# Kernel tuning notes

Hardware: AMD Instinct MI355X
Metric: run time of the kernel (lower is better)

Reference implementation:

```python
import jax, jax.numpy as jnp
import numpy as np
from jax import lax

B, T, V, E, H, K = 64, 512, 30000, 256, 256, 9


def setup_inputs() -> dict:
    key = jax.random.key(0)
    ks = jax.random.split(key, 15)
    s = 0.08
    return {
        "word_inputs": jax.random.randint(ks[0], (B, T), 0, V),
        "word_seq_lengths": jax.random.randint(ks[1], (B,), 1, T + 1),
        "seq_token_label": jax.random.randint(ks[2], (B, T), 0, K),
        "word_vec": jax.random.normal(ks[3], (V, E), jnp.float32) * s,
        "W_ih_f": jax.random.normal(ks[4], (4 * H, E), jnp.float32) * s,
        "W_hh_f": jax.random.normal(ks[5], (4 * H, H), jnp.float32) * s,
        "b_f": jax.random.normal(ks[6], (4 * H,), jnp.float32) * s,
        "W_ih_b": jax.random.normal(ks[7], (4 * H, E), jnp.float32) * s,
        "W_hh_b": jax.random.normal(ks[8], (4 * H, H), jnp.float32) * s,
        "b_b": jax.random.normal(ks[9], (4 * H,), jnp.float32) * s,
        "W_out": jax.random.normal(ks[10], (K, 2 * H), jnp.float32) * s,
        "b_out": jax.random.normal(ks[11], (K,), jnp.float32) * s,
        "start_trans": jax.random.normal(ks[12], (K,), jnp.float32) * s,
        "end_trans": jax.random.normal(ks[13], (K,), jnp.float32) * s,
        "trans": jax.random.normal(ks[14], (K, K), jnp.float32) * s,
    }


def _lstm_dir(x, W_ih, W_hh, b):
    # x: [B,T,E] -> h: [B,T,H]; torch gate order (i, f, g, o)
    gx = jnp.einsum('bte,ge->btg', x, W_ih) + b  # input projection hoisted out of scan
    h0 = jnp.zeros((x.shape[0], W_hh.shape[1]), x.dtype)

    def step(carry, g_t):
        h, c = carry
        g = g_t + h @ W_hh.T
        i, f, gg, o = jnp.split(g, 4, axis=-1)
        c = jax.nn.sigmoid(f) * c + jax.nn.sigmoid(i) * jnp.tanh(gg)
        h = jax.nn.sigmoid(o) * jnp.tanh(c)
        return (h, c), h

    _, hs = lax.scan(step, (h0, h0), jnp.swapaxes(gx, 0, 1))
    return jnp.swapaxes(hs, 0, 1)


def reference(word_inputs, word_seq_lengths, seq_token_label, word_vec,
              W_ih_f, W_hh_f, b_f, W_ih_b, W_hh_b, b_b,
              W_out, b_out, start_trans, end_trans, trans):
    t_idx = jnp.arange(T)
    mask = t_idx[None, :] < word_seq_lengths[:, None]  # [B,T] bool (pack_padded semantics)
    # index map that reverses the valid prefix of each sequence (involution)
    rev_idx = jnp.where(mask, word_seq_lengths[:, None] - 1 - t_idx[None, :], t_idx[None, :])

    emb = word_vec[word_inputs]  # [B,T,E]
    h_fwd = _lstm_dir(emb, W_ih_f, W_hh_f, b_f)
    emb_rev = jnp.take_along_axis(emb, rev_idx[:, :, None], axis=1)
    h_bwd = jnp.take_along_axis(_lstm_dir(emb_rev, W_ih_b, W_hh_b, b_b), rev_idx[:, :, None], axis=1)
    feats = jnp.concatenate([h_fwd, h_bwd], axis=-1) * mask[:, :, None]  # [B,T,2H]
    emissions = feats @ W_out.T + b_out  # [B,T,K]

    mf = mask.astype(emissions.dtype)
    # ---- CRF numerator (score of gold path) ----
    emit_sc = jnp.take_along_axis(emissions, seq_token_label[:, :, None], 2)[:, :, 0]  # [B,T]
    num = start_trans[seq_token_label[:, 0]] + emit_sc[:, 0]
    trans_sc = trans[seq_token_label[:, :-1], seq_token_label[:, 1:]]  # [B,T-1]
    num = num + jnp.sum((trans_sc + emit_sc[:, 1:]) * mf[:, 1:], axis=1)
    last_tags = jnp.take_along_axis(seq_token_label, (word_seq_lengths - 1)[:, None], 1)[:, 0]
    num = num + end_trans[last_tags]

    # ---- CRF log-partition (alpha recursion) ----
    em_t = jnp.swapaxes(emissions[:, 1:], 0, 1)  # [T-1,B,K]
    mk_t = jnp.swapaxes(mask[:, 1:], 0, 1)       # [T-1,B]
    score0 = start_trans[None, :] + emissions[:, 0]  # [B,K]

    def alpha_step(score, inp):
        e_t, m_t = inp
        nxt = jax.nn.logsumexp(score[:, :, None] + trans[None], axis=1) + e_t
        return jnp.where(m_t[:, None], nxt, score), None

    scoreZ, _ = lax.scan(alpha_step, score0, (em_t, mk_t))
    denom = jax.nn.logsumexp(scoreZ + end_trans[None, :], axis=1)
    ner_loss = -jnp.mean(num - denom)  # reduction='mean' over batch, negated

    # ---- Viterbi decode ----
    def vit_step(score, inp):
        e_t, m_t = inp
        tot = score[:, :, None] + trans[None]  # [B,K,K]
        best_prev = jnp.argmax(tot, axis=1)    # [B,K]
        nxt = jnp.max(tot, axis=1) + e_t
        return jnp.where(m_t[:, None], nxt, score), best_prev

    scoreV, hist = lax.scan(vit_step, score0, (em_t, mk_t))  # hist [T-1,B,K]
    best_last = jnp.argmax(scoreV + end_trans[None, :], axis=1)  # [B]

    def back_step(cur, inp):
        h_t, m_t = inp
        new = jnp.take_along_axis(h_t, cur[:, None], 1)[:, 0]
        cur = jnp.where(m_t, new, cur)
        return cur, cur

    _, preds_rev = lax.scan(back_step, best_last, (hist[::-1], mk_t[::-1]))  # [T-1,B]
    preds = jnp.concatenate([jnp.swapaxes(preds_rev[::-1], 0, 1), best_last[:, None]], axis=1)  # [B,T]
    preds = jnp.where(mask, preds, 0)

    return ner_loss, preds, feats
```

## Files before the change

kernel.cpp:

```cpp
#include <hip/hip_runtime.h>
#include <hip/hip_bf16.h>
#include <math.h>

#ifndef __has_builtin
#define __has_builtin(x) 0
#endif

typedef unsigned int uint;
typedef unsigned short ushort;
typedef _Float16 half2_t __attribute__((ext_vector_type(2)));

#define PREG 90
#define WREG_UINTS (PREG * 2 * 512)
#define WLDS_UINTS (19 * 512 * 4)

__device__ __forceinline__ float sigm(float x) {
    return __fdividef(1.0f, 1.0f + __expf(-x));
}
__device__ __forceinline__ float tanh_fast(float x) {
    float sg = __fdividef(1.0f, 1.0f + __expf(-2.0f * x));
    return sg + sg - 1.0f;
}
__device__ __forceinline__ float dot2f(uint w, uint h, float acc) {
#if __has_builtin(__builtin_amdgcn_fdot2)
    return __builtin_amdgcn_fdot2(__builtin_bit_cast(half2_t, w),
                                  __builtin_bit_cast(half2_t, h), acc, false);
#else
    half2_t a = __builtin_bit_cast(half2_t, w);
    half2_t b = __builtin_bit_cast(half2_t, h);
    return acc + (float)a.x * (float)b.x + (float)a.y * (float)b.y;
#endif
}
__device__ __forceinline__ uint packh2(float a, float b) {
    ushort u0 = __builtin_bit_cast(ushort, (_Float16)a);
    ushort u1 = __builtin_bit_cast(ushort, (_Float16)b);
    return (uint)u0 | ((uint)u1 << 16);
}

#define R90(X) \
  X(0) X(1) X(2) X(3) X(4) X(5) X(6) X(7) \
  X(8) X(9) X(10) X(11) X(12) X(13) X(14) X(15) \
  X(16) X(17) X(18) X(19) X(20) X(21) X(22) X(23) \
  X(24) X(25) X(26) X(27) X(28) X(29) X(30) X(31) \
  X(32) X(33) X(34) X(35) X(36) X(37) X(38) X(39) \
  X(40) X(41) X(42) X(43) X(44) X(45) X(46) X(47) \
  X(48) X(49) X(50) X(51) X(52) X(53) X(54) X(55) \
  X(56) X(57) X(58) X(59) X(60) X(61) X(62) X(63) \
  X(64) X(65) X(66) X(67) X(68) X(69) X(70) X(71) \
  X(72) X(73) X(74) X(75) X(76) X(77) X(78) X(79) \
  X(80) X(81) X(82) X(83) X(84) X(85) X(86) X(87) \
  X(88) X(89)

#define R19(X) \
  X(0) X(1) X(2) X(3) X(4) X(5) X(6) X(7) \
  X(8) X(9) X(10) X(11) X(12) X(13) X(14) X(15) \
  X(16) X(17) X(18)

#define WDECL(m) uint wA##m, wB##m;
#define WLOAD(m) wA##m = wreg[(2 * (m)) * 512 + tid]; \
                 wB##m = wreg[(2 * (m) + 1) * 512 + tid];
#define WSTEP(m) { \
    uint hp = (uint)__builtin_amdgcn_readlane((int)((m) < 64 ? r0 : r1), (m) & 63); \
    aA = dot2f(wA##m, hp, aA); \
    aB = dot2f(wB##m, hp, aB); }
#define LSTEP(i) { \
    uint4 w4 = reinterpret_cast<const uint4*>(lw)[((i) << 9) + tid]; \
    uint hp0 = (uint)__builtin_amdgcn_readlane((int)r1, 26 + 2 * (i)); \
    uint hp1 = (uint)__builtin_amdgcn_readlane((int)r1, 27 + 2 * (i)); \
    aA = dot2f(w4.x, hp0, aA); \
    aB = dot2f(w4.y, hp0, aB); \
    aA = dot2f(w4.z, hp1, aA); \
    aB = dot2f(w4.w, hp1, aB); }

__global__ __launch_bounds__(256) void zero_kernel(float* __restrict__ out,
                                                   const int* __restrict__ lens) {
    int bid = blockIdx.x;
    if (bid < 65536) {
        int g = bid * 256 + threadIdx.x;
        int row = g >> 9;
        int t = row & 511;
        int b = row >> 9;
        if (t >= lens[b]) out[32769 + g] = 0.0f;
    } else if (bid < 65536 + 128) {
        int p = (bid - 65536) * 256 + threadIdx.x;
        out[1 + p] = 0.0f;
    } else if (threadIdx.x == 0) {
        out[0] = 0.0f;
    }
}

__global__ __launch_bounds__(256) void pack_kernel(const float* __restrict__ WF,
                                                   const float* __restrict__ WB,
                                                   uint* __restrict__ wregF,
                                                   uint* __restrict__ wregB,
                                                   uint* __restrict__ wldsF,
                                                   uint* __restrict__ wldsB) {
    int id = blockIdx.x * 256 + threadIdx.x;
    const float* W = WF; uint* wr = wregF; uint* wl = wldsF;
    if (id >= 131072) { id -= 131072; W = WB; wr = wregB; wl = wldsB; }
    int m, x, tl, dst_lds = 0, id2 = 0;
    if (id < WREG_UINTS) {
        m = id >> 10;
        int r = id & 1023;
        x = r >> 9;
        tl = r & 511;
    } else {
        id2 = id - WREG_UINTS;
        int c = id2 & 3;
        int u = id2 >> 2;
        tl = u & 511;
        int g = u >> 9;
        m = PREG + 2 * g + (c >> 1);
        x = c & 1;
        dst_lds = 1;
    }
    int j = tl >> 1, s = tl & 1;
    int q = (s << 1) + x;
    const float* row = W + ((size_t)((q << 8) + j) << 8);
    uint pk = packh2(row[2 * m], row[2 * m + 1]);
    if (dst_lds) wl[id2] = pk;
    else         wr[((m << 1) + x) * 512 + tl] = pk;
}

__global__ __launch_bounds__(256) void wih_pack_kernel(const float* __restrict__ WihF,
                                                       const float* __restrict__ WihB,
                                                       uint* __restrict__ w16F,
                                                       uint* __restrict__ w16B) {
    int id = blockIdx.x * 256 + threadIdx.x;
    const float* W = WihF; uint* dst = w16F;
    if (id >= 131072) { id -= 131072; W = WihB; dst = w16B; }
    int col = id >> 7;
    int p = id & 127;
    int perm = ((col & 3) << 8) + (col >> 2);
    const float* row = W + ((size_t)perm << 8);
    dst[(col << 7) + p] = packh2(row[2 * p], row[2 * p + 1]);
}

__global__ __launch_bounds__(256) void gemm_gx_kernel(const int* __restrict__ widx,
                                                      const int* __restrict__ lens,
                                                      const float* __restrict__ wvec,
                                                      const uint* __restrict__ wih16,
                                                      const float* __restrict__ bias,
                                                      _Float16* __restrict__ gx) {
    int row0 = blockIdx.x * 64;
    int b = row0 >> 9;
    int t0 = row0 & 511;
    if (t0 >= lens[b]) return;
    int n0 = blockIdx.y * 64;

    __shared__ __align__(16) uint As[16][68];
    __shared__ __align__(16) uint Bs[16][68];
    __shared__ int aoff[64];

    int tid = threadIdx.x;
    if (tid < 64) aoff[tid] = widx[row0 + tid] << 8;
    __syncthreads();

    float acc[4][4] = {};
    int tn = tid & 15, tm = tid >> 4;

    for (int k0p = 0; k0p < 128; k0p += 16) {
#pragma unroll
        for (int p = 0; p < 4; ++p) {
            int lin = p * 256 + tid;
            int kp = lin & 15, m = lin >> 4;
            const float2 av = *reinterpret_cast<const float2*>(
                &wvec[aoff[m] + ((k0p + kp) << 1)]);
            As[kp][m] = packh2(av.x, av.y);
            Bs[kp][m] = wih16[((n0 + m) << 7) + k0p + kp];
        }
        __syncthreads();
#pragma unroll
        for (int kp = 0; kp < 16; ++kp) {
            uint4 a4 = *reinterpret_cast<const uint4*>(&As[kp][tm * 4]);
            uint4 b4 = *reinterpret_cast<const uint4*>(&Bs[kp][tn * 4]);
            uint am[4] = {a4.x, a4.y, a4.z, a4.w};
            uint bn[4] = {b4.x, b4.y, b4.z, b4.w};
#pragma unroll
            for (int i = 0; i < 4; ++i)
#pragma unroll
                for (int j = 0; j < 4; ++j) acc[i][j] = dot2f(am[i], bn[j], acc[i][j]);
        }
        __syncthreads();
    }

#pragma unroll
    for (int i = 0; i < 4; ++i) {
        int row = row0 + tm * 4 + i;
        ushort u[4];
#pragma unroll
        for (int j = 0; j < 4; ++j) {
            int col = n0 + tn * 4 + j;
            int perm = ((col & 3) << 8) + (col >> 2);
            u[j] = __builtin_bit_cast(ushort, (_Float16)(acc[i][j] + bias[perm]));
        }
        uint2 st;
        st.x = (uint)u[0] | ((uint)u[1] << 16);
        st.y = (uint)u[2] | ((uint)u[3] << 16);
        *reinterpret_cast<uint2*>(&gx[row * 1024 + n0 + tn * 4]) = st;
    }
}

__global__ __launch_bounds__(512, 1) void lstm_kernel(const _Float16* __restrict__ gx0,
                                                      const _Float16* __restrict__ gx1,
                                                      const uint* __restrict__ wreg0,
                                                      const uint* __restrict__ wreg1,
                                                      const uint* __restrict__ wlds0,
                                                      const uint* __restrict__ wlds1,
                                                      const int* __restrict__ lens,
                                                      float* __restrict__ feats) {
    int dir = blockIdx.x & 1;
    int b = blockIdx.x >> 1;
    const uint* gxu = reinterpret_cast<const uint*>(dir ? gx1 : gx0) + ((size_t)(b << 9) << 9);
    const uint* wreg = dir ? wreg1 : wreg0;
    const uint* wlds = dir ? wlds1 : wlds0;
    int len = lens[b];
    int tid = threadIdx.x;
    int lane = tid & 63;
    int sg = tid & 1;

    __shared__ __align__(16) uint lw[WLDS_UINTS];
    __shared__ __align__(16) uint hpair[2][128];

    for (int i = tid; i < WLDS_UINTS; i += 512) lw[i] = wlds[i];

    R90(WDECL)
    R90(WLOAD)
    __syncthreads();

    float c = 0.0f;
    uint r0 = 0, r1 = 0;
    int pp = 0;

    int t0i = dir ? (len - 1) : 0;
    uint g = gxu[(t0i << 9) + tid];

    for (int tp = 0; tp < len; ++tp) {
        int t = dir ? (len - 1 - tp) : tp;
        int tnn = dir ? (len - 2 - tp) : (tp + 1);
        tnn = tnn < 0 ? 0 : (tnn >= len ? len - 1 : tnn);
        uint gnext = gxu[(tnn << 9) + tid];

        half2_t gv = __builtin_bit_cast(half2_t, g);
        float aA = (float)gv.x;
        float aB = (float)gv.y;

        R90(WSTEP)
        R19(LSTEP)

        float y = sg ? aA + aA : aA;
        float sgm = __fdividef(1.0f, 1.0f + __expf(-y));
        float pA = sg ? sgm + sgm - 1.0f : sgm;
        float pB = sigm(aB);

        float oA = __shfl_xor(pA, 1);
        float oB = __shfl_xor(pB, 1);
        float si = sg ? oA : pA;
        float sf = sg ? oB : pB;
        float tg = sg ? pA : oA;
        float so = sg ? pB : oB;

        c = sf * c + si * tg;
        float h = so * tanh_fast(c);

        if (!sg) {
            reinterpret_cast<ushort*>(hpair[pp])[tid >> 1] =
                __builtin_bit_cast(ushort, (_Float16)h);
            feats[(size_t)(((b << 9) + t)) * 512 + (dir << 8) + (tid >> 1)] = h;
        }
        __syncthreads();
        r0 = hpair[pp][lane];
        r1 = hpair[pp][64 + lane];
        pp ^= 1;
        g = gnext;
    }
}

__global__ __launch_bounds__(64) void emis_kernel(const float* __restrict__ feats,
                                                  const float* __restrict__ Wout,
                                                  const float* __restrict__ bout,
                                                  const int* __restrict__ lens,
                                                  float* __restrict__ emis) {
    int r = blockIdx.x;
    int b = r >> 9, t = r & 511;
    if (t >= lens[b]) return;
    int lane = threadIdx.x;
    const float* fr = feats + (size_t)r * 512;
    float f[8];
#pragma unroll
    for (int i = 0; i < 8; ++i) f[i] = fr[i * 64 + lane];
#pragma unroll
    for (int k = 0; k < 9; ++k) {
        float p = 0.0f;
#pragma unroll
        for (int i = 0; i < 8; ++i) p = fmaf(f[i], Wout[k * 512 + i * 64 + lane], p);
#pragma unroll
        for (int off = 32; off; off >>= 1) p += __shfl_down(p, off);
        if (lane == 0) emis[r * 9 + k] = p + bout[k];
    }
}

__global__ __launch_bounds__(64) void crf_kernel(const float* __restrict__ emis,
                                                 const int* __restrict__ lens,
                                                 const int* __restrict__ labels,
                                                 const float* __restrict__ start_trans,
                                                 const float* __restrict__ end_trans,
                                                 const float* __restrict__ trans,
                                                 float* __restrict__ out) {
    int b = blockIdx.x;
    int len = lens[b];
    int lane = threadIdx.x;
    __shared__ float alpha[9], vit[9];
    __shared__ unsigned char hist[512 * 9];
    const float* eb = emis + b * 512 * 9;
    const int* lb = labels + b * 512;

    float tr[9];
    if (lane < 9) {
#pragma unroll
        for (int i = 0; i < 9; ++i) tr[i] = trans[i * 9 + lane];
        float s0 = start_trans[lane] + eb[lane];
        alpha[lane] = s0;
        vit[lane] = s0;
    }
    __syncthreads();

    for (int t = 1; t < len; ++t) {
        float na = 0.0f, nv = 0.0f;
        if (lane < 9) {
            float e = eb[t * 9 + lane];
            float a[9];
#pragma unroll
            for (int i = 0; i < 9; ++i) a[i] = alpha[i] + tr[i];
            float m = a[0];
#pragma unroll
            for (int i = 1; i < 9; ++i) m = fmaxf(m, a[i]);
            float s = 0.0f;
#pragma unroll
            for (int i = 0; i < 9; ++i) s += __expf(a[i] - m);
            na = m + __logf(s) + e;
            float bv = vit[0] + tr[0];
            int bi = 0;
#pragma unroll
            for (int i = 1; i < 9; ++i) {
                float x = vit[i] + tr[i];
                if (x > bv) { bv = x; bi = i; }
            }
            nv = bv + e;
            hist[t * 9 + lane] = (unsigned char)bi;
        }
        __syncthreads();
        if (lane < 9) { alpha[lane] = na; vit[lane] = nv; }
        __syncthreads();
    }

    float part = 0.0f;
    for (int t = 1 + lane; t < len; t += 64) {
        int yp = lb[t - 1], y = lb[t];
        part += trans[yp * 9 + y] + eb[t * 9 + y];
    }
#pragma unroll
    for (int off = 32; off; off >>= 1) part += __shfl_down(part, off);

    if (lane == 0) {
        int y0 = lb[0];
        float num = start_trans[y0] + eb[y0] + part + end_trans[lb[len - 1]];
        float m = alpha[0] + end_trans[0];
        for (int j = 1; j < 9; ++j) m = fmaxf(m, alpha[j] + end_trans[j]);
        float s = 0.0f;
        for (int j = 0; j < 9; ++j) s += __expf(alpha[j] + end_trans[j] - m);
        float denom = m + __logf(s);
        atomicAdd(out, (denom - num) * (1.0f / 64.0f));

        float bm = vit[0] + end_trans[0];
        int cur = 0;
        for (int j = 1; j < 9; ++j) {
            float x = vit[j] + end_trans[j];
            if (x > bm) { bm = x; cur = j; }
        }
        float* preds = out + 1 + b * 512;
        preds[len - 1] = (float)cur;
        for (int t = len - 1; t >= 1; --t) {
            cur = hist[t * 9 + cur];
            preds[t - 1] = (float)cur;
        }
    }
}

extern "C" void kernel_launch(void* const* d_in, const int* in_sizes, int n_in,
                              void* d_out, int out_size, void* d_ws, size_t ws_size,
                              hipStream_t stream) {
    const int* widx = (const int*)d_in[0];
    const int* lens = (const int*)d_in[1];
    const int* labels = (const int*)d_in[2];
    const float* wvec = (const float*)d_in[3];
    const float* WihF = (const float*)d_in[4];
    const float* WhhF = (const float*)d_in[5];
    const float* bF = (const float*)d_in[6];
    const float* WihB = (const float*)d_in[7];
    const float* WhhB = (const float*)d_in[8];
    const float* bB = (const float*)d_in[9];
    const float* Wout = (const float*)d_in[10];
    const float* bout = (const float*)d_in[11];
    const float* start_trans = (const float*)d_in[12];
    const float* end_trans = (const float*)d_in[13];
    const float* trans9 = (const float*)d_in[14];
    float* out = (float*)d_out;
    char* ws = (char*)d_ws;

    _Float16* gxF = (_Float16*)(ws);
    _Float16* gxB = (_Float16*)(ws + 67108864);
    uint* wregF   = (uint*)(ws + 134217728);
    uint* wregB   = (uint*)(ws + 134586368);
    uint* wldsF   = (uint*)(ws + 134955008);
    uint* wldsB   = (uint*)(ws + 135110656);
    uint* wih16F  = (uint*)(ws + 135266304);
    uint* wih16B  = (uint*)(ws + 135790592);
    float* emis   = (float*)(ws + 135266304);
    (void)in_sizes; (void)n_in; (void)out_size; (void)ws_size;

    float* feats = out + 1 + 32768;

    zero_kernel<<<65665, 256, 0, stream>>>(out, lens);
    pack_kernel<<<1024, 256, 0, stream>>>(WhhF, WhhB, wregF, wregB, wldsF, wldsB);
    wih_pack_kernel<<<1024, 256, 0, stream>>>(WihF, WihB, wih16F, wih16B);

    dim3 ggrid(512, 16);
    gemm_gx_kernel<<<ggrid, 256, 0, stream>>>(widx, lens, wvec, wih16F, bF, gxF);
    gemm_gx_kernel<<<ggrid, 256, 0, stream>>>(widx, lens, wvec, wih16B, bB, gxB);

    lstm_kernel<<<128, 512, 0, stream>>>(gxF, gxB, wregF, wregB, wldsF, wldsB, lens, feats);

    emis_kernel<<<32768, 64, 0, stream>>>(feats, Wout, bout, lens, emis);
    crf_kernel<<<64, 64, 0, stream>>>(emis, lens, labels, start_trans, end_trans, trans9, out);
}
```

Before: 1.652 ms.

## Hold recurrent weights in AGPRs and run two LSTM blocks per CU

The 180 register-resident W_hh fp16 pairs per thread are moved from VGPRs into accumulation registers (AGPRs) via inline asm. Launch bounds are raised to 2 blocks per SM, so two batch/direction LSTM recurrences can share a compute unit. The weight pack layout is interleaved so each thread loads an A/B pair with one uint2 load. Each dot2 accumulator chain is also split in two to cut serial dependency. The risks are the extra accvgpr_read per weight on every step, possible register spills under the tighter budget, and pressure on the LDS weight cache once two blocks share it.

```diff
diff --git a/kernel.cpp b/kernel.cpp
--- a/kernel.cpp
+++ b/kernel.cpp
@@ -56,21 +56,26 @@
   X(8) X(9) X(10) X(11) X(12) X(13) X(14) X(15) \
   X(16) X(17) X(18)
 
-#define WDECL(m) uint wA##m, wB##m;
-#define WLOAD(m) wA##m = wreg[(2 * (m)) * 512 + tid]; \
-                 wB##m = wreg[(2 * (m) + 1) * 512 + tid];
+#define WDECL(m) uint wa##m, wb##m;
+#define WLOAD(m) { \
+    uint2 t = wp2[(m) * 512 + tid]; \
+    asm volatile("v_accvgpr_write_b32 %0, %1" : "=a"(wa##m) : "v"(t.x)); \
+    asm volatile("v_accvgpr_write_b32 %0, %1" : "=a"(wb##m) : "v"(t.y)); }
 #define WSTEP(m) { \
     uint hp = (uint)__builtin_amdgcn_readlane((int)((m) < 64 ? r0 : r1), (m) & 63); \
-    aA = dot2f(wA##m, hp, aA); \
-    aB = dot2f(wB##m, hp, aB); }
+    uint va, vb; \
+    asm volatile("v_accvgpr_read_b32 %0, %1" : "=v"(va) : "a"(wa##m)); \
+    asm volatile("v_accvgpr_read_b32 %0, %1" : "=v"(vb) : "a"(wb##m)); \
+    if ((m) & 1) { aA1 = dot2f(va, hp, aA1); aB1 = dot2f(vb, hp, aB1); } \
+    else         { aA0 = dot2f(va, hp, aA0); aB0 = dot2f(vb, hp, aB0); } }
 #define LSTEP(i) { \
     uint4 w4 = reinterpret_cast<const uint4*>(lw)[((i) << 9) + tid]; \
     uint hp0 = (uint)__builtin_amdgcn_readlane((int)r1, 26 + 2 * (i)); \
     uint hp1 = (uint)__builtin_amdgcn_readlane((int)r1, 27 + 2 * (i)); \
-    aA = dot2f(w4.x, hp0, aA); \
-    aB = dot2f(w4.y, hp0, aB); \
-    aA = dot2f(w4.z, hp1, aA); \
-    aB = dot2f(w4.w, hp1, aB); }
+    aA0 = dot2f(w4.x, hp0, aA0); \
+    aB0 = dot2f(w4.y, hp0, aB0); \
+    aA1 = dot2f(w4.z, hp1, aA1); \
+    aB1 = dot2f(w4.w, hp1, aB1); }
 
 __global__ __launch_bounds__(256) void zero_kernel(float* __restrict__ out,
                                                    const int* __restrict__ lens) {
@@ -102,8 +107,8 @@
     if (id < WREG_UINTS) {
         m = id >> 10;
         int r = id & 1023;
-        x = r >> 9;
-        tl = r & 511;
+        tl = r >> 1;
+        x = r & 1;
     } else {
         id2 = id - WREG_UINTS;
         int c = id2 & 3;
@@ -119,7 +124,7 @@
     const float* row = W + ((size_t)((q << 8) + j) << 8);
     uint pk = packh2(row[2 * m], row[2 * m + 1]);
     if (dst_lds) wl[id2] = pk;
-    else         wr[((m << 1) + x) * 512 + tl] = pk;
+    else         wr[(m << 10) + (tl << 1) + x] = pk;
 }
 
 __global__ __launch_bounds__(256) void wih_pack_kernel(const float* __restrict__ WihF,
@@ -201,7 +206,7 @@
     }
 }
 
-__global__ __launch_bounds__(512, 1) void lstm_kernel(const _Float16* __restrict__ gx0,
+__global__ __launch_bounds__(512, 2) void lstm_kernel(const _Float16* __restrict__ gx0,
                                                       const _Float16* __restrict__ gx1,
                                                       const uint* __restrict__ wreg0,
                                                       const uint* __restrict__ wreg1,
@@ -214,6 +219,7 @@
     const uint* gxu = reinterpret_cast<const uint*>(dir ? gx1 : gx0) + ((size_t)(b << 9) << 9);
     const uint* wreg = dir ? wreg1 : wreg0;
     const uint* wlds = dir ? wlds1 : wlds0;
+    const uint2* wp2 = reinterpret_cast<const uint2*>(wreg);
     int len = lens[b];
     int tid = threadIdx.x;
     int lane = tid & 63;
@@ -242,11 +248,14 @@
         uint gnext = gxu[(tnn << 9) + tid];
 
         half2_t gv = __builtin_bit_cast(half2_t, g);
-        float aA = (float)gv.x;
-        float aB = (float)gv.y;
+        float aA0 = (float)gv.x, aA1 = 0.0f;
+        float aB0 = (float)gv.y, aB1 = 0.0f;
 
         R90(WSTEP)
         R19(LSTEP)
+
+        float aA = aA0 + aA1;
+        float aB = aB0 + aB1;
 
         float y = sg ? aA + aA : aA;
         float sgm = __fdividef(1.0f, 1.0f + __expf(-y));
```

Measured after the change: 2.000 ms. 1.21x slower.
